# Kernel optimization log

Measured on AMD Instinct MI355X. Metric: run time of the kernel, lower is better.

Reference implementation:

```python
import jax, jax.numpy as jnp
import numpy as np

NEG_SLOPE = 0.2


def _gat(x, W, a_src, a_dst, bias, src, dst, nonself, N):
    # PyG GATConv (eval mode): h = x @ W -> [N,H,C]; per-edge scores with
    # LeakyReLU, softmax over incoming edges per target node (self loops
    # re-added after removing any existing ones), weighted scatter-add.
    H, C = a_src.shape
    h = (x @ W).reshape(N, H, C)
    al_s = jnp.einsum('nhc,hc->nh', h, a_src)  # [N,H]
    al_d = jnp.einsum('nhc,hc->nh', h, a_dst)
    e = jax.nn.leaky_relu(al_s[src] + al_d[dst], NEG_SLOPE)  # [E,H]
    e = jnp.where(nonself[:, None], e, -jnp.inf)  # drop input self loops
    e_self = jax.nn.leaky_relu(al_s + al_d, NEG_SLOPE)  # added self loops [N,H]
    m = jnp.maximum(jax.ops.segment_max(e, dst, num_segments=N), e_self)
    w = jnp.exp(e - m[dst])  # masked edges -> 0
    w_self = jnp.exp(e_self - m)
    num = jax.ops.segment_sum(w[:, :, None] * h[src], dst, num_segments=N)
    num = num + w_self[:, :, None] * h
    den = jax.ops.segment_sum(w, dst, num_segments=N) + w_self
    return (num / den[:, :, None]).reshape(N, H * C) + bias


def setup_inputs() -> dict:
    N, E = 100000, 3200000
    key = jax.random.key(0)
    ks = jax.random.split(key, 20)
    s = 0.1
    return {
        'x1': jax.random.normal(ks[0], (N, 7), jnp.float32),
        'x2': jax.random.normal(ks[1], (N, 1), jnp.float32),
        'edge_index': jax.random.randint(ks[2], (2, E), 0, N, jnp.int64)
            if jax.config.jax_enable_x64 else jax.random.randint(ks[2], (2, E), 0, N, jnp.int32),
        'num_nodes': N,
        'lin1_w': s * jax.random.normal(ks[3], (1, 7), jnp.float32),
        'lin1_b': s * jax.random.normal(ks[4], (1,), jnp.float32),
        'lin2_w': s * jax.random.normal(ks[5], (1, 8), jnp.float32),
        'W1': s * jax.random.normal(ks[6], (1, 32), jnp.float32),
        'a_src1': s * jax.random.normal(ks[7], (8, 4), jnp.float32),
        'a_dst1': s * jax.random.normal(ks[8], (8, 4), jnp.float32),
        'b1': s * jax.random.normal(ks[9], (32,), jnp.float32),
        'W2': s * jax.random.normal(ks[10], (32, 16), jnp.float32),
        'a_src2': s * jax.random.normal(ks[11], (4, 4), jnp.float32),
        'a_dst2': s * jax.random.normal(ks[12], (4, 4), jnp.float32),
        'b2': s * jax.random.normal(ks[13], (16,), jnp.float32),
        'W3': s * jax.random.normal(ks[14], (16, 8), jnp.float32),
        'a_src3': s * jax.random.normal(ks[15], (2, 4), jnp.float32),
        'a_dst3': s * jax.random.normal(ks[16], (2, 4), jnp.float32),
        'b3': s * jax.random.normal(ks[17], (8,), jnp.float32),
    }


def reference(x1, x2, edge_index, num_nodes, lin1_w, lin1_b, lin2_w,
              W1, a_src1, a_dst1, b1, W2, a_src2, a_dst2, b2,
              W3, a_src3, a_dst3, b3):
    N = num_nodes
    src, dst = edge_index[0], edge_index[1]
    nonself = src != dst
    # init score + 3 GAT layers (dropouts inactive in eval mode)
    h0 = jax.nn.relu(x1 @ lin1_w.T + lin1_b)  # [N,1]
    x3 = jax.nn.relu(_gat(h0, W1, a_src1, a_dst1, b1, src, dst, nonself, N))
    x4 = jax.nn.relu(_gat(x3, W2, a_src2, a_dst2, b2, src, dst, nonself, N))
    x6 = jax.nn.relu(_gat(x4, W3, a_src3, a_dst3, b3, src, dst, nonself, N))  # [N,8]
    # Row-normalized adjacency with diagonal filled to 1 (sparse form of the
    # original dense Adj): Adj[i,j] = 1/deg[i] on edges (i!=j) and diagonal.
    ns = nonself.astype(x6.dtype)
    deg = 1.0 + jax.ops.segment_sum(ns, src, num_segments=N)  # [N]
    # local score: rowsum(Adj * (x6 x6^T))
    dots = jnp.sum(x6[src] * x6[dst], axis=-1) * ns  # [E]
    local = (jax.ops.segment_sum(dots, src, num_segments=N)
             + jnp.sum(x6 * x6, axis=-1)) / deg  # [N]
    # global score: lin2(Adj @ x6)
    R3 = (jax.ops.segment_sum(x6[dst] * ns[:, None], src, num_segments=N)
          + x6) / deg[:, None]  # [N,8]
    return local[:, None] + R3 @ lin2_w.T  # [N,1]
```

## Files before the change

### kernel.cpp

```cpp
#include <hip/hip_runtime.h>
#include <hip/hip_fp16.h>
#include <math.h>

static constexpr float NEG_SLOPE = 0.2f;
static constexpr int P      = 256;
static constexpr int CAP    = 14000;
static constexpr int CHSZ   = 4096;

__device__ __forceinline__ float lrelu(float x) { return x > 0.0f ? x : NEG_SLOPE * x; }

__device__ __forceinline__ void dm(int x, unsigned int mg, int npr, int& r, int& lk) {
    r = (int)__umulhi((unsigned int)x, mg);
    lk = x - r * npr;
    if (lk >= npr) { lk -= npr; ++r; }
    else if (lk < 0) { lk += npr; --r; }
}

union H8 { int4 i4; __half2 h2[4]; };

__device__ __forceinline__ void h8_to_f(int4 v, float* o) {
    H8 u; u.i4 = v;
#pragma unroll
    for (int k = 0; k < 4; ++k) {
        float2 f = __half22float2(u.h2[k]);
        o[2 * k] = f.x; o[2 * k + 1] = f.y;
    }
}

__device__ __forceinline__ int4 f_to_h8(const float* s) {
    H8 u;
#pragma unroll
    for (int k = 0; k < 4; ++k)
        u.h2[k] = __float22half2_rn(make_float2(s[2 * k], s[2 * k + 1]));
    return u.i4;
}

__global__ __launch_bounds__(512) void part2_kernel(
    const int* __restrict__ src, const int* __restrict__ dst,
    int* __restrict__ gcount,
    unsigned int* __restrict__ stgd, unsigned int* __restrict__ stgs,
    int E, int npr, unsigned int mg)
{
    __shared__ int cntw[8 * P];
    __shared__ int base[P];
    __shared__ int pref[P];
    __shared__ int wsum[8];
    __shared__ unsigned int buf[CHSZ];
    __shared__ unsigned char rid[CHSZ];
    const int dir = blockIdx.x & 1;
    const int c = blockIdx.x >> 1;
    const int i0 = c * CHSZ;
    const int i1 = min(i0 + CHSZ, E);
    const int tot = i1 - i0;
    const int tid = threadIdx.x;
    const int lane = tid & 63, w = tid >> 6;
    const int* key = dir ? (src + i0) : (dst + i0);
    const int* val = dir ? (dst + i0) : (src + i0);
    unsigned int* stg = dir ? stgs : stgd;
    int* gc = gcount + dir * P;
    int* mycnt = cntw + w * P;
    for (int i = tid; i < 8 * P; i += 512) cntw[i] = 0;
    __syncthreads();
    const int nv = tot >> 2;
    const int4* k4 = (const int4*)key;
    for (int t = tid; t < nv; t += 512) {
        int4 k = k4[t];
        int r, lk;
        dm(k.x, mg, npr, r, lk); atomicAdd(&mycnt[r], 1);
        dm(k.y, mg, npr, r, lk); atomicAdd(&mycnt[r], 1);
        dm(k.z, mg, npr, r, lk); atomicAdd(&mycnt[r], 1);
        dm(k.w, mg, npr, r, lk); atomicAdd(&mycnt[r], 1);
    }
    for (int i = (nv << 2) + tid; i < tot; i += 512) {
        int r, lk;
        dm(key[i], mg, npr, r, lk);
        atomicAdd(&mycnt[r], 1);
    }
    __syncthreads();
    int cq[8];
    int tb = 0, x = 0;
    if (tid < P) {
#pragma unroll
        for (int q = 0; q < 8; ++q) { cq[q] = cntw[q * P + tid]; tb += cq[q]; }
        base[tid] = atomicAdd(&gc[tid], tb);
        x = tb;
#pragma unroll
        for (int off = 1; off < 64; off <<= 1) {
            int y = __shfl_up(x, off);
            if (lane >= off) x += y;
        }
        if (lane == 63) wsum[w] = x;
    }
    __syncthreads();
    if (tid < P) {
        int wpref = 0;
#pragma unroll
        for (int k = 0; k < 4; ++k) if (k < w) wpref += wsum[k];
        int ex = x + wpref - tb;
        pref[tid] = ex;
        int acc = ex;
#pragma unroll
        for (int q = 0; q < 8; ++q) { cntw[q * P + tid] = acc; acc += cq[q]; }
    }
    __syncthreads();
    int* mytick = cntw + w * P;
    for (int t = tid; t < nv; t += 512) {
        int4 k = k4[t];
        const int4* v4 = (const int4*)val;
        int4 v = v4[t];
        int r, lk, p;
        dm(k.x, mg, npr, r, lk); p = atomicAdd(&mytick[r], 1);
        buf[p] = ((unsigned int)lk << 17) | (unsigned int)v.x; rid[p] = (unsigned char)r;
        dm(k.y, mg, npr, r, lk); p = atomicAdd(&mytick[r], 1);
        buf[p] = ((unsigned int)lk << 17) | (unsigned int)v.y; rid[p] = (unsigned char)r;
        dm(k.z, mg, npr, r, lk); p = atomicAdd(&mytick[r], 1);
        buf[p] = ((unsigned int)lk << 17) | (unsigned int)v.z; rid[p] = (unsigned char)r;
        dm(k.w, mg, npr, r, lk); p = atomicAdd(&mytick[r], 1);
        buf[p] = ((unsigned int)lk << 17) | (unsigned int)v.w; rid[p] = (unsigned char)r;
    }
    for (int i = (nv << 2) + tid; i < tot; i += 512) {
        int r, lk;
        dm(key[i], mg, npr, r, lk);
        int p = atomicAdd(&mytick[r], 1);
        buf[p] = ((unsigned int)lk << 17) | (unsigned int)val[i];
        rid[p] = (unsigned char)r;
    }
    __syncthreads();
    for (int i = tid; i < tot; i += 512) {
        int r = (int)rid[i];
        int b = base[r] + (i - pref[r]);
        if (b < CAP) stg[(size_t)r * CAP + b] = buf[i];
    }
}

__global__ __launch_bounds__(512) void ebase_kernel(
    const int* __restrict__ gtot, int* __restrict__ ebase)
{
    __shared__ int sm[2 * P];
    int tid = threadIdx.x;
    int v = gtot[tid];
    sm[tid] = v;
    __syncthreads();
#pragma unroll
    for (int off = 1; off < P; off <<= 1) {
        int t = ((tid & (P - 1)) >= off) ? sm[tid - off] : 0;
        __syncthreads();
        sm[tid] += t;
        __syncthreads();
    }
    ebase[tid] = sm[tid] - v;
}

__global__ __launch_bounds__(512) void build_kernel(
    const unsigned int* __restrict__ stgd, const unsigned int* __restrict__ stgs,
    const int* __restrict__ gtot, const int* __restrict__ ebase,
    int* __restrict__ col_dst, int* __restrict__ col_src,
    int* __restrict__ deg_dst, int* __restrict__ deg_src,
    int* __restrict__ row_dst, int* __restrict__ row_src,
    int N, int npr)
{
    __shared__ int cntw[2 * 512];
    __shared__ int scn[512];
    __shared__ int outv[CAP];
    const int dir = blockIdx.x >> 8;
    const int r = blockIdx.x & (P - 1);
    const unsigned int* stg = (dir ? stgs : stgd) + (size_t)r * CAP;
    int tot = gtot[dir * P + r];
    if (tot > CAP) tot = CAP;
    const int n0 = r * npr;
    const int nb = min(npr, N - n0);
    const int tid = threadIdx.x;
    const int g = tid >> 8;
    int* mycnt = cntw + g * 512;
    cntw[tid] = 0; cntw[512 + tid] = 0;
    __syncthreads();
    for (int i = tid; i < tot; i += 512)
        atomicAdd(&mycnt[stg[i] >> 17], 1);
    __syncthreads();
    int c0 = cntw[tid], c1 = cntw[512 + tid];
    int v = c0 + c1;
    scn[tid] = v;
    __syncthreads();
#pragma unroll
    for (int off = 1; off < 512; off <<= 1) {
        int t = (tid >= off) ? scn[tid - off] : 0;
        __syncthreads();
        scn[tid] += t;
        __syncthreads();
    }
    int ex = scn[tid] - v;
    const int eb = ebase[dir * P + r];
    if (tid < nb) {
        (dir ? deg_src : deg_dst)[n0 + tid] = v;
        (dir ? row_src : row_dst)[n0 + tid] = eb + ex;
    }
    cntw[tid] = ex;
    cntw[512 + tid] = ex + c0;
    __syncthreads();
    for (int i = tid; i < tot; i += 512) {
        unsigned int w = stg[i];
        int t = atomicAdd(&mycnt[w >> 17], 1);
        unsigned int vv = w & 0x1FFFFu;
        unsigned int self = (vv == (unsigned int)(n0) + (w >> 17)) ? 0x80000000u : 0u;
        outv[t] = (int)(vv | self);
    }
    __syncthreads();
    int* col = (dir ? col_src : col_dst) + eb;
    for (int i = tid; i < tot; i += 512) col[i] = outv[i];
}

__global__ __launch_bounds__(256) void l1h0_kernel(
    const float* __restrict__ x1, const float* __restrict__ lin1_w,
    const float* __restrict__ lin1_b, float* __restrict__ h0, int N)
{
    int n = blockIdx.x * blockDim.x + threadIdx.x;
    if (n >= N) return;
    float acc = lin1_b[0];
#pragma unroll
    for (int k = 0; k < 7; ++k) acc = fmaf(x1[n * 7 + k], lin1_w[k], acc);
    h0[n] = fmaxf(acc, 0.0f);
}

__global__ __launch_bounds__(256) void expand_kernel(
    const int* __restrict__ col, const float* __restrict__ h0,
    float* __restrict__ colh0, int E)
{
    int t = blockIdx.x * 256 + threadIdx.x;
    int e0 = t * 4;
    if (e0 + 3 < E) {
        int4 c = *(const int4*)(col + e0);
        float4 v;
        v.x = (c.x < 0) ? -1.0f : h0[c.x & 0x7fffffff];
        v.y = (c.y < 0) ? -1.0f : h0[c.y & 0x7fffffff];
        v.z = (c.z < 0) ? -1.0f : h0[c.z & 0x7fffffff];
        v.w = (c.w < 0) ? -1.0f : h0[c.w & 0x7fffffff];
        *(float4*)(colh0 + e0) = v;
    } else {
        for (int e = e0; e < E; ++e) {
            int c = col[e];
            colh0[e] = (c < 0) ? -1.0f : h0[c & 0x7fffffff];
        }
    }
}

__global__ __launch_bounds__(256) void gat_gather1_kernel(
    const int* __restrict__ row_start, const int* __restrict__ degv,
    const float* __restrict__ colh0, const float* __restrict__ h0,
    const float* __restrict__ W1, const float* __restrict__ a_src,
    const float* __restrict__ a_dst, const float* __restrict__ bias,
    const float* __restrict__ W2, int4* __restrict__ h2p, int N)
{
    int t = blockIdx.x * 256 + threadIdx.x;
    int n = t >> 3, lane = t & 7;
    if (n >= N) return;
    float cs[8], cd[8];
#pragma unroll
    for (int hd = 0; hd < 8; ++hd) {
        float s = 0.0f, d = 0.0f;
#pragma unroll
        for (int c = 0; c < 4; ++c) {
            s = fmaf(W1[hd * 4 + c], a_src[hd * 4 + c], s);
            d = fmaf(W1[hd * 4 + c], a_dst[hd * 4 + c], d);
        }
        cs[hd] = s; cd[hd] = d;
    }
    float h0n = h0[n];
    float wh[8], den[8], adn[8];
#pragma unroll
    for (int hd = 0; hd < 8; ++hd) {
        adn[hd] = h0n * cd[hd];
        if (lane == 0) {
            float w = __expf(lrelu(h0n * cs[hd] + adn[hd]));
            den[hd] = w; wh[hd] = w * h0n;
        } else { den[hd] = 0.0f; wh[hd] = 0.0f; }
    }
    int start = row_start[n];
    int end = start + degv[n];
    int e = start + lane;
    for (; e + 8 < end; e += 16) {
        float a0 = colh0[e];
        float a1 = colh0[e + 8];
        if (a0 >= 0.0f) {
#pragma unroll
            for (int hd = 0; hd < 8; ++hd) {
                float w = __expf(lrelu(a0 * cs[hd] + adn[hd]));
                den[hd] += w;
                wh[hd] = fmaf(w, a0, wh[hd]);
            }
        }
        if (a1 >= 0.0f) {
#pragma unroll
            for (int hd = 0; hd < 8; ++hd) {
                float w = __expf(lrelu(a1 * cs[hd] + adn[hd]));
                den[hd] += w;
                wh[hd] = fmaf(w, a1, wh[hd]);
            }
        }
    }
    if (e < end) {
        float a0 = colh0[e];
        if (a0 >= 0.0f) {
#pragma unroll
            for (int hd = 0; hd < 8; ++hd) {
                float w = __expf(lrelu(a0 * cs[hd] + adn[hd]));
                den[hd] += w;
                wh[hd] = fmaf(w, a0, wh[hd]);
            }
        }
    }
#pragma unroll
    for (int m = 1; m < 8; m <<= 1) {
#pragma unroll
        for (int hd = 0; hd < 8; ++hd) {
            den[hd] += __shfl_xor(den[hd], m);
            wh[hd]  += __shfl_xor(wh[hd], m);
        }
    }
    float fct = wh[lane] / den[lane];
    const float4 wv = ((const float4*)W1)[lane];
    const float4 bb = ((const float4*)bias)[lane];
    float xr[4];
    xr[0] = fmaxf(fmaf(fct, wv.x, bb.x), 0.0f);
    xr[1] = fmaxf(fmaf(fct, wv.y, bb.y), 0.0f);
    xr[2] = fmaxf(fmaf(fct, wv.z, bb.z), 0.0f);
    xr[3] = fmaxf(fmaf(fct, wv.w, bb.w), 0.0f);
    float pj[16];
#pragma unroll
    for (int j = 0; j < 16; ++j) pj[j] = 0.0f;
    const float* wbase = W2 + lane * 64;
#pragma unroll
    for (int c2 = 0; c2 < 4; ++c2) {
#pragma unroll
        for (int j = 0; j < 16; ++j)
            pj[j] = fmaf(xr[c2], wbase[c2 * 16 + j], pj[j]);
    }
#pragma unroll
    for (int m = 1; m < 8; m <<= 1) {
#pragma unroll
        for (int j = 0; j < 16; ++j) pj[j] += __shfl_xor(pj[j], m);
    }
    if (lane < 2) h2p[(size_t)n * 2 + lane] = f_to_h8(pj + lane * 8);
}

__device__ __forceinline__ void g2_acc(
    const float* hs, const float* As, const float* ald, float* num, float* den)
{
#pragma unroll
    for (int hd = 0; hd < 4; ++hd) {
        float a = 0.0f;
#pragma unroll
        for (int c = 0; c < 4; ++c) a = fmaf(hs[hd * 4 + c], As[hd * 4 + c], a);
        float w = __expf(lrelu(a + ald[hd]));
        den[hd] += w;
#pragma unroll
        for (int c = 0; c < 4; ++c) num[hd * 4 + c] = fmaf(w, hs[hd * 4 + c], num[hd * 4 + c]);
    }
}

__global__ __launch_bounds__(256) void gat_gather2_kernel(
    const int* __restrict__ row_start, const int* __restrict__ degv,
    const int* __restrict__ col, const int4* __restrict__ hp,
    const float* __restrict__ a_src, const float* __restrict__ a_dst,
    const float* __restrict__ bias, const float* __restrict__ W3,
    int4* __restrict__ h3p, int N)
{
    int t = blockIdx.x * 256 + threadIdx.x;
    int n = t >> 3, lane = t & 7;
    if (n >= N) return;
    float As[16], Ad[16];
#pragma unroll
    for (int j = 0; j < 16; ++j) { As[j] = a_src[j]; Ad[j] = a_dst[j]; }
    float hn[16];
    h8_to_f(hp[(size_t)n * 2], hn);
    h8_to_f(hp[(size_t)n * 2 + 1], hn + 8);
    float ald[4];
#pragma unroll
    for (int hd = 0; hd < 4; ++hd) {
        float d = 0.0f;
#pragma unroll
        for (int c = 0; c < 4; ++c) d = fmaf(hn[hd * 4 + c], Ad[hd * 4 + c], d);
        ald[hd] = d;
    }
    float num[16], den[4];
    if (lane == 0) {
#pragma unroll
        for (int hd = 0; hd < 4; ++hd) {
            float a = 0.0f;
#pragma unroll
            for (int c = 0; c < 4; ++c) a = fmaf(hn[hd * 4 + c], As[hd * 4 + c], a);
            float w = __expf(lrelu(a + ald[hd]));
            den[hd] = w;
#pragma unroll
            for (int c = 0; c < 4; ++c) num[hd * 4 + c] = w * hn[hd * 4 + c];
        }
    } else {
#pragma unroll
        for (int j = 0; j < 16; ++j) num[j] = 0.0f;
#pragma unroll
        for (int hd = 0; hd < 4; ++hd) den[hd] = 0.0f;
    }
    int start = row_start[n];
    int end = start + degv[n];
    int e = start + lane;
    for (; e + 8 < end; e += 16) {
        int s0 = col[e], s1 = col[e + 8];
        int i0 = s0 & 0x7fffffff, i1 = s1 & 0x7fffffff;
        int4 q00 = hp[(size_t)i0 * 2], q01 = hp[(size_t)i0 * 2 + 1];
        int4 q10 = hp[(size_t)i1 * 2], q11 = hp[(size_t)i1 * 2 + 1];
        if (s0 >= 0) {
            float hs[16];
            h8_to_f(q00, hs); h8_to_f(q01, hs + 8);
            g2_acc(hs, As, ald, num, den);
        }
        if (s1 >= 0) {
            float hs[16];
            h8_to_f(q10, hs); h8_to_f(q11, hs + 8);
            g2_acc(hs, As, ald, num, den);
        }
    }
    if (e < end) {
        int s0 = col[e];
        if (s0 >= 0) {
            float hs[16];
            h8_to_f(hp[(size_t)s0 * 2], hs);
            h8_to_f(hp[(size_t)s0 * 2 + 1], hs + 8);
            g2_acc(hs, As, ald, num, den);
        }
    }
#pragma unroll
    for (int m = 1; m < 8; m <<= 1) {
#pragma unroll
        for (int hd = 0; hd < 4; ++hd) den[hd] += __shfl_xor(den[hd], m);
#pragma unroll
        for (int j = 0; j < 16; ++j) num[j] += __shfl_xor(num[j], m);
    }
    float invd[4];
#pragma unroll
    for (int hd = 0; hd < 4; ++hd) invd[hd] = 1.0f / den[hd];
    float pj[8];
#pragma unroll
    for (int j = 0; j < 8; ++j) pj[j] = 0.0f;
#pragma unroll
    for (int k = 0; k < 16; ++k) {
        float xk = fmaxf(fmaf(num[k], invd[k >> 2], bias[k]), 0.0f);
        const float* wrow = W3 + k * 8;
#pragma unroll
        for (int j = 0; j < 8; ++j) pj[j] = fmaf(xk, wrow[j], pj[j]);
    }
    if (lane == 0) h3p[n] = f_to_h8(pj);
}

__device__ __forceinline__ void g3_acc(
    const float* hs, const float* As, const float* ald, float* num, float* den)
{
#pragma unroll
    for (int hd = 0; hd < 2; ++hd) {
        float a = 0.0f;
#pragma unroll
        for (int c = 0; c < 4; ++c) a = fmaf(hs[hd * 4 + c], As[hd * 4 + c], a);
        float w = __expf(lrelu(a + ald[hd]));
        den[hd] += w;
#pragma unroll
        for (int c = 0; c < 4; ++c) num[hd * 4 + c] = fmaf(w, hs[hd * 4 + c], num[hd * 4 + c]);
    }
}

__global__ __launch_bounds__(256) void gat_gather3_kernel(
    const int* __restrict__ row_start, const int* __restrict__ degv,
    const int* __restrict__ col, const int4* __restrict__ hp,
    const float* __restrict__ a_src, const float* __restrict__ a_dst,
    const float* __restrict__ bias, int4* __restrict__ x6p, int N)
{
    int t = blockIdx.x * 256 + threadIdx.x;
    int n = t >> 2, lane = t & 3;
    if (n >= N) return;
    float As[8], Ad[8];
#pragma unroll
    for (int j = 0; j < 8; ++j) { As[j] = a_src[j]; Ad[j] = a_dst[j]; }
    float hn[8];
    h8_to_f(hp[n], hn);
    float ald[2];
#pragma unroll
    for (int hd = 0; hd < 2; ++hd) {
        float d = 0.0f;
#pragma unroll
        for (int c = 0; c < 4; ++c) d = fmaf(hn[hd * 4 + c], Ad[hd * 4 + c], d);
        ald[hd] = d;
    }
    float num[8], den[2];
    if (lane == 0) {
#pragma unroll
        for (int hd = 0; hd < 2; ++hd) {
            float a = 0.0f;
#pragma unroll
            for (int c = 0; c < 4; ++c) a = fmaf(hn[hd * 4 + c], As[hd * 4 + c], a);
            float w = __expf(lrelu(a + ald[hd]));
            den[hd] = w;
#pragma unroll
            for (int c = 0; c < 4; ++c) num[hd * 4 + c] = w * hn[hd * 4 + c];
        }
    } else {
#pragma unroll
        for (int j = 0; j < 8; ++j) num[j] = 0.0f;
        den[0] = den[1] = 0.0f;
    }
    int start = row_start[n];
    int end = start + degv[n];
    int e = start + lane;
    for (; e + 4 < end; e += 8) {
        int s0 = col[e], s1 = col[e + 4];
        int i0 = s0 & 0x7fffffff, i1 = s1 & 0x7fffffff;
        int4 q0 = hp[i0], q1 = hp[i1];
        if (s0 >= 0) {
            float hs[8];
            h8_to_f(q0, hs);
            g3_acc(hs, As, ald, num, den);
        }
        if (s1 >= 0) {
            float hs[8];
            h8_to_f(q1, hs);
            g3_acc(hs, As, ald, num, den);
        }
    }
    if (e < end) {
        int s0 = col[e];
        if (s0 >= 0) {
            float hs[8];
            h8_to_f(hp[s0], hs);
            g3_acc(hs, As, ald, num, den);
        }
    }
#pragma unroll
    for (int m = 1; m < 4; m <<= 1) {
        den[0] += __shfl_xor(den[0], m);
        den[1] += __shfl_xor(den[1], m);
#pragma unroll
        for (int j = 0; j < 8; ++j) num[j] += __shfl_xor(num[j], m);
    }
    if (lane == 0) {
        float o[8];
        float i0 = 1.0f / den[0], i1 = 1.0f / den[1];
#pragma unroll
        for (int c = 0; c < 4; ++c) {
            o[c]     = fmaxf(fmaf(num[c], i0, bias[c]), 0.0f);
            o[4 + c] = fmaxf(fmaf(num[4 + c], i1, bias[4 + c]), 0.0f);
        }
        x6p[n] = f_to_h8(o);
    }
}

__global__ __launch_bounds__(256) void score_gather_kernel(
    const int* __restrict__ row_start, const int* __restrict__ degv,
    const int* __restrict__ col, const int4* __restrict__ x6p,
    const float* __restrict__ lin2_w, float* __restrict__ out, int N)
{
    int t = blockIdx.x * 256 + threadIdx.x;
    int n = t >> 2, lane = t & 3;
    if (n >= N) return;
    float sx[8];
    h8_to_f(x6p[n], sx);
    float r[8];
    int sc = 0;
    if (lane == 0) {
#pragma unroll
        for (int j = 0; j < 8; ++j) r[j] = sx[j];
    } else {
#pragma unroll
        for (int j = 0; j < 8; ++j) r[j] = 0.0f;
    }
    int start = row_start[n];
    int dg = degv[n];
    int end = start + dg;
    int e = start + lane;
    for (; e + 4 < end; e += 8) {
        int d0 = col[e], d1 = col[e + 4];
        int i0 = d0 & 0x7fffffff, i1 = d1 & 0x7fffffff;
        int4 q0 = x6p[i0], q1 = x6p[i1];
        if (d0 < 0) { ++sc; }
        else {
            float dx[8];
            h8_to_f(q0, dx);
#pragma unroll
            for (int j = 0; j < 8; ++j) r[j] += dx[j];
        }
        if (d1 < 0) { ++sc; }
        else {
            float dx[8];
            h8_to_f(q1, dx);
#pragma unroll
            for (int j = 0; j < 8; ++j) r[j] += dx[j];
        }
    }
    if (e < end) {
        int d0 = col[e];
        if (d0 < 0) { ++sc; }
        else {
            float dx[8];
            h8_to_f(x6p[d0], dx);
#pragma unroll
            for (int j = 0; j < 8; ++j) r[j] += dx[j];
        }
    }
#pragma unroll
    for (int m = 1; m < 4; m <<= 1) {
        sc += __shfl_xor(sc, m);
#pragma unroll
        for (int j = 0; j < 8; ++j) r[j] += __shfl_xor(r[j], m);
    }
    if (lane == 0) {
        float invd = 1.0f / (1.0f + (float)(dg - sc));
        float loc = 0.0f, g = 0.0f;
#pragma unroll
        for (int j = 0; j < 8; ++j) {
            loc = fmaf(sx[j], r[j], loc);
            g   = fmaf(r[j], lin2_w[j], g);
        }
        out[n] = (loc + g) * invd;
    }
}

extern "C" void kernel_launch(void* const* d_in, const int* in_sizes, int n_in,
                              void* d_out, int out_size, void* d_ws, size_t ws_size,
                              hipStream_t stream)
{
    const float* x1     = (const float*)d_in[0];
    const int*   ei     = (const int*)d_in[2];
    const float* lin1_w = (const float*)d_in[4];
    const float* lin1_b = (const float*)d_in[5];
    const float* lin2_w = (const float*)d_in[6];
    const float* W1     = (const float*)d_in[7];
    const float* a_src1 = (const float*)d_in[8];
    const float* a_dst1 = (const float*)d_in[9];
    const float* b1     = (const float*)d_in[10];
    const float* W2     = (const float*)d_in[11];
    const float* a_src2 = (const float*)d_in[12];
    const float* a_dst2 = (const float*)d_in[13];
    const float* b2     = (const float*)d_in[14];
    const float* W3     = (const float*)d_in[15];
    const float* a_src3 = (const float*)d_in[16];
    const float* a_dst3 = (const float*)d_in[17];
    const float* b3     = (const float*)d_in[18];
    float* out = (float*)d_out;

    const int N = in_sizes[0] / 7;
    const int E = in_sizes[2] / 2;
    const int* src = ei;
    const int* dst = ei + E;

    const int npr = (N + P - 1) / P;
    const unsigned int mg = (unsigned int)((0x100000000ULL + npr - 1) / (unsigned long long)npr);
    const int PB = (E + CHSZ - 1) / CHSZ;

    size_t Ns = (size_t)N, Es = (size_t)E;
    int* ideg_dst = (int*)d_ws;
    int* ideg_src = ideg_dst + Ns;
    int* irow_dst = ideg_src + Ns;
    int* irow_src = irow_dst + Ns;
    int* gcount   = irow_src + Ns;
    int* iebase   = gcount + 2 * P;
    int* icol_dst = iebase + 2 * P;
    int* icol_src = icol_dst + Es;
    float* f = (float*)(icol_src + Es);
    unsigned int* stgd = (unsigned int*)f;
    unsigned int* stgs = stgd + (size_t)P * CAP;
    float* h0    = f;
    int4*  h2p   = (int4*)(f + Ns);
    int4*  h3p   = (int4*)(f + 9 * Ns);
    int4*  x6p   = (int4*)(f + 13 * Ns);
    float* colh0 = f + 17 * Ns;

    const int TB = 256;
    const int gN  = (N + TB - 1) / TB;
    const int g8  = (8 * N + TB - 1) / TB;
    const int g4  = (4 * N + TB - 1) / TB;
    const int gE4 = (E / 4 + TB - 1) / TB;

    hipMemsetAsync(gcount, 0, 2 * P * sizeof(int), stream);
    part2_kernel<<<2 * PB, 512, 0, stream>>>(src, dst, gcount, stgd, stgs, E, npr, mg);
    ebase_kernel<<<1, 2 * P, 0, stream>>>(gcount, iebase);
    build_kernel<<<2 * P, 512, 0, stream>>>(stgd, stgs, gcount, iebase,
                                            icol_dst, icol_src,
                                            ideg_dst, ideg_src,
                                            irow_dst, irow_src, N, npr);

    l1h0_kernel<<<gN, TB, 0, stream>>>(x1, lin1_w, lin1_b, h0, N);
    expand_kernel<<<gE4, TB, 0, stream>>>(icol_dst, h0, colh0, E);
    gat_gather1_kernel<<<g8, TB, 0, stream>>>(irow_dst, ideg_dst, colh0,
                                              h0, W1, a_src1, a_dst1, b1, W2, h2p, N);

    gat_gather2_kernel<<<g8, TB, 0, stream>>>(irow_dst, ideg_dst, icol_dst,
                                              h2p, a_src2, a_dst2, b2, W3, h3p, N);

    gat_gather3_kernel<<<g4, TB, 0, stream>>>(irow_dst, ideg_dst, icol_dst,
                                              h3p, a_src3, a_dst3, b3, x6p, N);

    score_gather_kernel<<<g4, TB, 0, stream>>>(irow_src, ideg_src, icol_src,
                                               x6p, lin2_w, out, N);
}
```

Baseline: 274.8 us.

## Fold ebase scan and h0 expansion into build kernel; widen gather lanes

The separate ebase prefix-scan kernel is removed. Each build block now computes its own base offset with a wave-reduction over the preceding partition totals, and its in-block scan is replaced by a shuffle-based wave scan instead of a 9-step shared-memory scan with barriers. The expand kernel is fused into the build kernel's dst-direction writeback, which writes colh0 alongside col_dst. To support this, h0 is computed first and moved to a buffer region that does not alias the staging buffers. Layer-3 GAT and score gathers now use 8 lanes per node instead of 4, which adds parallelism per node at the cost of more shuffle reduction steps.

```diff
diff --git a/kernel.cpp b/kernel.cpp
--- a/kernel.cpp
+++ b/kernel.cpp
@@ -133,34 +133,18 @@
     }
 }
 
-__global__ __launch_bounds__(512) void ebase_kernel(
-    const int* __restrict__ gtot, int* __restrict__ ebase)
-{
-    __shared__ int sm[2 * P];
-    int tid = threadIdx.x;
-    int v = gtot[tid];
-    sm[tid] = v;
-    __syncthreads();
-#pragma unroll
-    for (int off = 1; off < P; off <<= 1) {
-        int t = ((tid & (P - 1)) >= off) ? sm[tid - off] : 0;
-        __syncthreads();
-        sm[tid] += t;
-        __syncthreads();
-    }
-    ebase[tid] = sm[tid] - v;
-}
-
 __global__ __launch_bounds__(512) void build_kernel(
     const unsigned int* __restrict__ stgd, const unsigned int* __restrict__ stgs,
-    const int* __restrict__ gtot, const int* __restrict__ ebase,
+    const int* __restrict__ gtot,
+    const float* __restrict__ h0, float* __restrict__ colh0,
     int* __restrict__ col_dst, int* __restrict__ col_src,
     int* __restrict__ deg_dst, int* __restrict__ deg_src,
     int* __restrict__ row_dst, int* __restrict__ row_src,
     int N, int npr)
 {
     __shared__ int cntw[2 * 512];
-    __shared__ int scn[512];
+    __shared__ int wtmp[8];
+    __shared__ int s_eb;
     __shared__ int outv[CAP];
     const int dir = blockIdx.x >> 8;
     const int r = blockIdx.x & (P - 1);
@@ -170,26 +154,44 @@
     const int n0 = r * npr;
     const int nb = min(npr, N - n0);
     const int tid = threadIdx.x;
+    const int lane = tid & 63, w = tid >> 6;
     const int g = tid >> 8;
     int* mycnt = cntw + g * 512;
     cntw[tid] = 0; cntw[512 + tid] = 0;
-    __syncthreads();
+    int contrib = (tid < r) ? gtot[dir * P + tid] : 0;
+    int rsum = contrib;
+#pragma unroll
+    for (int off = 1; off < 64; off <<= 1) rsum += __shfl_xor(rsum, off);
+    if (lane == 0) wtmp[w] = rsum;
+    __syncthreads();
+    if (tid == 0) {
+        int a = 0;
+#pragma unroll
+        for (int k = 0; k < 8; ++k) a += wtmp[k];
+        s_eb = a;
+    }
+    __syncthreads();
+    const int eb = s_eb;
     for (int i = tid; i < tot; i += 512)
         atomicAdd(&mycnt[stg[i] >> 17], 1);
     __syncthreads();
     int c0 = cntw[tid], c1 = cntw[512 + tid];
     int v = c0 + c1;
-    scn[tid] = v;
-    __syncthreads();
-#pragma unroll
-    for (int off = 1; off < 512; off <<= 1) {
-        int t = (tid >= off) ? scn[tid - off] : 0;
-        __syncthreads();
-        scn[tid] += t;
-        __syncthreads();
-    }
-    int ex = scn[tid] - v;
-    const int eb = ebase[dir * P + r];
+    int x = v;
+#pragma unroll
+    for (int off = 1; off < 64; off <<= 1) {
+        int y = __shfl_up(x, off);
+        if (lane >= off) x += y;
+    }
+    if (lane == 63) wtmp[w] = x;
+    __syncthreads();
+    if (tid == 0) {
+        int a = 0;
+#pragma unroll
+        for (int k = 0; k < 8; ++k) { int t2 = wtmp[k]; wtmp[k] = a; a += t2; }
+    }
+    __syncthreads();
+    int ex = x + wtmp[w] - v;
     if (tid < nb) {
         (dir ? deg_src : deg_dst)[n0 + tid] = v;
         (dir ? row_src : row_dst)[n0 + tid] = eb + ex;
@@ -198,15 +200,25 @@
     cntw[512 + tid] = ex + c0;
     __syncthreads();
     for (int i = tid; i < tot; i += 512) {
-        unsigned int w = stg[i];
-        int t = atomicAdd(&mycnt[w >> 17], 1);
-        unsigned int vv = w & 0x1FFFFu;
-        unsigned int self = (vv == (unsigned int)(n0) + (w >> 17)) ? 0x80000000u : 0u;
+        unsigned int wv = stg[i];
+        int t = atomicAdd(&mycnt[wv >> 17], 1);
+        unsigned int vv = wv & 0x1FFFFu;
+        unsigned int self = (vv == (unsigned int)(n0) + (wv >> 17)) ? 0x80000000u : 0u;
         outv[t] = (int)(vv | self);
     }
     __syncthreads();
-    int* col = (dir ? col_src : col_dst) + eb;
-    for (int i = tid; i < tot; i += 512) col[i] = outv[i];
+    if (dir == 0) {
+        int* col = col_dst + eb;
+        float* ch = colh0 + eb;
+        for (int i = tid; i < tot; i += 512) {
+            int vv = outv[i];
+            col[i] = vv;
+            ch[i] = (vv < 0) ? -1.0f : h0[vv];
+        }
+    } else {
+        int* col = col_src + eb;
+        for (int i = tid; i < tot; i += 512) col[i] = outv[i];
+    }
 }
 
 __global__ __launch_bounds__(256) void l1h0_kernel(
@@ -219,28 +231,6 @@
 #pragma unroll
     for (int k = 0; k < 7; ++k) acc = fmaf(x1[n * 7 + k], lin1_w[k], acc);
     h0[n] = fmaxf(acc, 0.0f);
-}
-
-__global__ __launch_bounds__(256) void expand_kernel(
-    const int* __restrict__ col, const float* __restrict__ h0,
-    float* __restrict__ colh0, int E)
-{
-    int t = blockIdx.x * 256 + threadIdx.x;
-    int e0 = t * 4;
-    if (e0 + 3 < E) {
-        int4 c = *(const int4*)(col + e0);
-        float4 v;
-        v.x = (c.x < 0) ? -1.0f : h0[c.x & 0x7fffffff];
-        v.y = (c.y < 0) ? -1.0f : h0[c.y & 0x7fffffff];
-        v.z = (c.z < 0) ? -1.0f : h0[c.z & 0x7fffffff];
-        v.w = (c.w < 0) ? -1.0f : h0[c.w & 0x7fffffff];
-        *(float4*)(colh0 + e0) = v;
-    } else {
-        for (int e = e0; e < E; ++e) {
-            int c = col[e];
-            colh0[e] = (c < 0) ? -1.0f : h0[c & 0x7fffffff];
-        }
-    }
 }
 
 __global__ __launch_bounds__(256) void gat_gather1_kernel(
@@ -422,8 +412,8 @@
         int s0 = col[e];
         if (s0 >= 0) {
             float hs[16];
-            h8_to_f(hp[(size_t)s0 * 2], hs);
-            h8_to_f(hp[(size_t)s0 * 2 + 1], hs + 8);
+            h8_to_f(hp[(size_t)(s0 & 0x7fffffff) * 2], hs);
+            h8_to_f(hp[(size_t)(s0 & 0x7fffffff) * 2 + 1], hs + 8);
             g2_acc(hs, As, ald, num, den);
         }
     }
@@ -472,7 +462,7 @@
     const float* __restrict__ bias, int4* __restrict__ x6p, int N)
 {
     int t = blockIdx.x * 256 + threadIdx.x;
-    int n = t >> 2, lane = t & 3;
+    int n = t >> 3, lane = t & 7;
     if (n >= N) return;
     float As[8], Ad[8];
 #pragma unroll
@@ -507,8 +497,8 @@
     int start = row_start[n];
     int end = start + degv[n];
     int e = start + lane;
-    for (; e + 4 < end; e += 8) {
-        int s0 = col[e], s1 = col[e + 4];
+    for (; e + 8 < end; e += 16) {
+        int s0 = col[e], s1 = col[e + 8];
         int i0 = s0 & 0x7fffffff, i1 = s1 & 0x7fffffff;
         int4 q0 = hp[i0], q1 = hp[i1];
         if (s0 >= 0) {
@@ -526,12 +516,12 @@
         int s0 = col[e];
         if (s0 >= 0) {
             float hs[8];
-            h8_to_f(hp[s0], hs);
+            h8_to_f(hp[s0 & 0x7fffffff], hs);
             g3_acc(hs, As, ald, num, den);
         }
     }
 #pragma unroll
-    for (int m = 1; m < 4; m <<= 1) {
+    for (int m = 1; m < 8; m <<= 1) {
         den[0] += __shfl_xor(den[0], m);
         den[1] += __shfl_xor(den[1], m);
 #pragma unroll
@@ -555,7 +545,7 @@
     const float* __restrict__ lin2_w, float* __restrict__ out, int N)
 {
     int t = blockIdx.x * 256 + threadIdx.x;
-    int n = t >> 2, lane = t & 3;
+    int n = t >> 3, lane = t & 7;
     if (n >= N) return;
     float sx[8];
     h8_to_f(x6p[n], sx);
@@ -572,8 +562,8 @@
     int dg = degv[n];
     int end = start + dg;
     int e = start + lane;
-    for (; e + 4 < end; e += 8) {
-        int d0 = col[e], d1 = col[e + 4];
+    for (; e + 8 < end; e += 16) {
+        int d0 = col[e], d1 = col[e + 8];
         int i0 = d0 & 0x7fffffff, i1 = d1 & 0x7fffffff;
         int4 q0 = x6p[i0], q1 = x6p[i1];
         if (d0 < 0) { ++sc; }
@@ -596,13 +586,13 @@
         if (d0 < 0) { ++sc; }
         else {
             float dx[8];
-            h8_to_f(x6p[d0], dx);
+            h8_to_f(x6p[d0 & 0x7fffffff], dx);
 #pragma unroll
             for (int j = 0; j < 8; ++j) r[j] += dx[j];
         }
     }
 #pragma unroll
-    for (int m = 1; m < 4; m <<= 1) {
+    for (int m = 1; m < 8; m <<= 1) {
         sc += __shfl_xor(sc, m);
 #pragma unroll
         for (int j = 0; j < 8; ++j) r[j] += __shfl_xor(r[j], m);
@@ -657,43 +647,39 @@
     int* irow_dst = ideg_src + Ns;
     int* irow_src = irow_dst + Ns;
     int* gcount   = irow_src + Ns;
-    int* iebase   = gcount + 2 * P;
-    int* icol_dst = iebase + 2 * P;
+    int* icol_dst = gcount + 2 * P;
     int* icol_src = icol_dst + Es;
     float* f = (float*)(icol_src + Es);
     unsigned int* stgd = (unsigned int*)f;
     unsigned int* stgs = stgd + (size_t)P * CAP;
-    float* h0    = f;
-    int4*  h2p   = (int4*)(f + Ns);
-    int4*  h3p   = (int4*)(f + 9 * Ns);
-    int4*  x6p   = (int4*)(f + 13 * Ns);
-    float* colh0 = f + 17 * Ns;
+    float* h0    = f + 72 * Ns;
+    float* colh0 = f + 73 * Ns;
+    int4*  h2p   = (int4*)f;
+    int4*  h3p   = (int4*)(f + 8 * Ns);
+    int4*  x6p   = (int4*)(f + 12 * Ns);
 
     const int TB = 256;
     const int gN  = (N + TB - 1) / TB;
     const int g8  = (8 * N + TB - 1) / TB;
-    const int g4  = (4 * N + TB - 1) / TB;
-    const int gE4 = (E / 4 + TB - 1) / TB;
+
+    l1h0_kernel<<<gN, TB, 0, stream>>>(x1, lin1_w, lin1_b, h0, N);
 
     hipMemsetAsync(gcount, 0, 2 * P * sizeof(int), stream);
     part2_kernel<<<2 * PB, 512, 0, stream>>>(src, dst, gcount, stgd, stgs, E, npr, mg);
-    ebase_kernel<<<1, 2 * P, 0, stream>>>(gcount, iebase);
-    build_kernel<<<2 * P, 512, 0, stream>>>(stgd, stgs, gcount, iebase,
+    build_kernel<<<2 * P, 512, 0, stream>>>(stgd, stgs, gcount, h0, colh0,
                                             icol_dst, icol_src,
                                             ideg_dst, ideg_src,
                                             irow_dst, irow_src, N, npr);
 
-    l1h0_kernel<<<gN, TB, 0, stream>>>(x1, lin1_w, lin1_b, h0, N);
-    expand_kernel<<<gE4, TB, 0, stream>>>(icol_dst, h0, colh0, E);
     gat_gather1_kernel<<<g8, TB, 0, stream>>>(irow_dst, ideg_dst, colh0,
                                               h0, W1, a_src1, a_dst1, b1, W2, h2p, N);
 
     gat_gather2_kernel<<<g8, TB, 0, stream>>>(irow_dst, ideg_dst, icol_dst,
                                               h2p, a_src2, a_dst2, b2, W3, h3p, N);
 
-    gat_gather3_kernel<<<g4, TB, 0, stream>>>(irow_dst, ideg_dst, icol_dst,
+    gat_gather3_kernel<<<g8, TB, 0, stream>>>(irow_dst, ideg_dst, icol_dst,
                                               h3p, a_src3, a_dst3, b3, x6p, N);
 
-    score_gather_kernel<<<g4, TB, 0, stream>>>(irow_src, ideg_src, icol_src,
+    score_gather_kernel<<<g8, TB, 0, stream>>>(irow_src, ideg_src, icol_src,
                                                x6p, lin2_w, out, N);
 }
```

Result: faster. 261.9 us (-4.7%).
